# Kernel optimization log

Hardware: AMD Instinct MI355X
Metric: run time of the kernel (lower is better)

The kernel has to match this reference:

```python
import jax, jax.numpy as jnp
import numpy as np

B, S, H = 1, 4096, 3584
NQ, NKV, D = 16, 8, 256
N_REP = NQ // NKV  # GQA repeat factor = 2
WINDOW = 2048
SOFTCAP = 50.0
THETA = 10000.0
SCALE = D ** -0.5


def rotate_half(x):
    h = x.shape[-1] // 2
    return jnp.concatenate([-x[..., h:], x[..., :h]], axis=-1)


def setup_inputs() -> dict:
    key = jax.random.key(0)
    k0, k1, k2, k3, k4 = jax.random.split(key, 5)
    return {
        "hidden_states": jax.random.normal(k0, (B, S, H), jnp.float32),
        "wq": jax.random.normal(k1, (H, NQ * D), jnp.float32) / np.sqrt(H).astype(np.float32),
        "wk": jax.random.normal(k2, (H, NKV * D), jnp.float32) / np.sqrt(H).astype(np.float32),
        "wv": jax.random.normal(k3, (H, NKV * D), jnp.float32) / np.sqrt(H).astype(np.float32),
        "wo": jax.random.normal(k4, (NQ * D, H), jnp.float32) / np.sqrt(NQ * D).astype(np.float32),
        "position_ids": jnp.arange(S, dtype=jnp.int64 if jax.config.jax_enable_x64 else jnp.int32)[None, :],
    }


def reference(hidden_states, wq, wk, wv, wo, position_ids):
    b, s, h = hidden_states.shape
    # QKV projections (no bias, per attention_bias=False)
    q = (hidden_states @ wq).reshape(b, s, NQ, D).transpose(0, 2, 1, 3)   # [b, nq, s, d]
    k = (hidden_states @ wk).reshape(b, s, NKV, D).transpose(0, 2, 1, 3)  # [b, nkv, s, d]
    v = (hidden_states @ wv).reshape(b, s, NKV, D).transpose(0, 2, 1, 3)

    # Rotary embeddings (Gemma2RotaryEmbedding): freqs duplicated, rotate_half form
    pos = position_ids.astype(jnp.float32)                         # [b, s]
    inv_freq = 1.0 / (THETA ** (jnp.arange(0, D, 2, dtype=jnp.float32) / D))  # [d/2]
    freqs = pos[..., None] * inv_freq                              # [b, s, d/2]
    emb = jnp.concatenate([freqs, freqs], axis=-1)                 # [b, s, d]
    cos = jnp.cos(emb)[:, None, :, :]                              # [b, 1, s, d]
    sin = jnp.sin(emb)[:, None, :, :]
    q = q * cos + rotate_half(q) * sin
    k = k * cos + rotate_half(k) * sin

    # GQA: repeat_kv (repeat_interleave over head dim)
    k = jnp.repeat(k, N_REP, axis=1)  # [b, nq, s, d]
    v = jnp.repeat(v, N_REP, axis=1)

    # scaled scores + logit softcapping
    scores = jnp.einsum('bhqd,bhkd->bhqk', q, k) * SCALE
    scores = SOFTCAP * jnp.tanh(scores / SOFTCAP)

    # causal + sliding-window mask built from positions
    qpos = position_ids[:, None, :, None]  # [b,1,s,1]
    kpos = position_ids[:, None, None, :]  # [b,1,1,s]
    visible = (kpos <= qpos) & (kpos > qpos - WINDOW)
    scores = jnp.where(visible, scores, jnp.finfo(scores.dtype).min)

    attn = jax.nn.softmax(scores, axis=-1)
    out = jnp.einsum('bhqk,bhkd->bhqd', attn, v)      # [b, nq, s, d]
    out = out.transpose(0, 2, 1, 3).reshape(b, s, NQ * D)
    return out @ wo                                    # [b, s, h]
```

## Files before the change

### kernel.cpp

```cpp
#include <hip/hip_runtime.h>
#include <hip/hip_bf16.h>
#include <cstdint>
#include <cstddef>

#define DEVFN __device__ __forceinline__

typedef __attribute__((ext_vector_type(4))) float f32x4;
typedef __attribute__((ext_vector_type(8))) short bf16x8;
typedef __attribute__((ext_vector_type(4))) short short4v;
typedef __attribute__((ext_vector_type(8))) short short8v;

static constexpr int S = 4096;
static constexpr int H = 3584;
static constexpr int NQ = 16;
static constexpr int NKV = 8;
static constexpr int D = 256;
static constexpr int WINDOW = 2048;
static constexpr float SCALE = 0.0625f;

DEVFN unsigned short f2bf(float f) {
  union { float f; uint32_t u; } x; x.f = f;
  uint32_t u = x.u;
  u += 0x7fffu + ((u >> 16) & 1u);
  return (unsigned short)(u >> 16);
}
DEVFN float bf2f(unsigned short h) {
  union { uint32_t u; float f; } x; x.u = ((uint32_t)h) << 16;
  return x.f;
}

DEVFN void load_lds16(const void* g, void* l) {
  __builtin_amdgcn_global_load_lds((const __attribute__((address_space(1))) void*)g,
                                   (__attribute__((address_space(3))) void*)l,
                                   16, 0, 0);
}

__global__ __launch_bounds__(256) void cast_hs_kernel(const float* __restrict__ in,
                                                      unsigned short* __restrict__ out) {
  int i = (blockIdx.x * 256 + threadIdx.x) * 8;
  float4 a = *(const float4*)(in + i);
  float4 b = *(const float4*)(in + i + 4);
  short8v o;
  o[0] = (short)f2bf(a.x); o[1] = (short)f2bf(a.y);
  o[2] = (short)f2bf(a.z); o[3] = (short)f2bf(a.w);
  o[4] = (short)f2bf(b.x); o[5] = (short)f2bf(b.y);
  o[6] = (short)f2bf(b.z); o[7] = (short)f2bf(b.w);
  *(short8v*)(out + i) = o;
}

__global__ __launch_bounds__(256) void transpose_cast_kernel(const float* __restrict__ in,
                                                             unsigned short* __restrict__ out,
                                                             int rows, int cols, int out_ld) {
  __shared__ float tile[64][65];
  const int r0 = blockIdx.y * 64, c0 = blockIdx.x * 64;
  const int t = threadIdx.x;
  const int rr = t >> 4, c4 = (t & 15) * 4;
#pragma unroll
  for (int j = 0; j < 4; ++j) {
    float4 v = *(const float4*)(in + (size_t)(r0 + rr + j * 16) * cols + c0 + c4);
    tile[rr + j * 16][c4 + 0] = v.x;
    tile[rr + j * 16][c4 + 1] = v.y;
    tile[rr + j * 16][c4 + 2] = v.z;
    tile[rr + j * 16][c4 + 3] = v.w;
  }
  __syncthreads();
  const int c = t >> 2, ch = (t & 3) * 16;
  short8v o0, o1;
#pragma unroll
  for (int j = 0; j < 8; ++j) o0[j] = (short)f2bf(tile[ch + j][c]);
#pragma unroll
  for (int j = 0; j < 8; ++j) o1[j] = (short)f2bf(tile[ch + 8 + j][c]);
  unsigned short* dst = out + (size_t)(c0 + c) * out_ld + r0 + ch;
  *(short8v*)dst = o0;
  *(short8v*)(dst + 8) = o1;
}

__global__ __launch_bounds__(256) void rope_table_kernel(float* __restrict__ cs) {
  int idx = blockIdx.x * 256 + threadIdx.x;
  int s = idx >> 7, i = idx & 127;
  float inv = exp2f((float)i * -0.10381025296523007f);
  float f = (float)s * inv;
  cs[idx] = cosf(f);
  cs[(S * 128) + idx] = sinf(f);
}

DEVFN void gemm256_mainloop(const unsigned short* __restrict__ A,
                            const unsigned short* __restrict__ Bt,
                            int Kdim, int lda, int ldb, int row0, int col0,
                            char* lds, f32x4 acc[8][4]) {
  const int tid = threadIdx.x, lane = tid & 63;
  const int w = tid >> 6;
  const int wm = w >> 2, wn = w & 3;
  const int NT = Kdim >> 6;

  const int u = ((tid & 7) * 16) ^ (((tid >> 3) & 7) << 4);
  const int srow = (tid >> 3) + (u >> 6) * 128;
  const int sc = (u & 63) >> 1;

  const unsigned short* aSrc = A + (size_t)(row0 + srow) * lda + sc;
  const unsigned short* bSrc = Bt + (size_t)(col0 + srow) * ldb + sc;
  const size_t aj = (size_t)64 * lda, bj = (size_t)64 * ldb;

  char* const dA = lds + tid * 16;
  char* const dB = lds + 32768 + tid * 16;

  const int aoff = (lane & 15) * 128 + ((((lane >> 4) * 16) + wm * 64) ^ ((lane & 7) << 4));
  int boffs[4];
#pragma unroll
  for (int n = 0; n < 4; ++n)
    boffs[n] = (wn >> 1) * 8192 + ((wn & 1) * 32 + (n & 1) * 16 + (lane & 15)) * 128 +
               ((((lane >> 4) | ((n >> 1) << 2)) ^ (lane & 7)) << 4);

#define STAGE_A(kt2, kh) do { \
    char* d_ = dA + (((kt2) & 1) << 16) + ((kh) << 14); \
    const unsigned short* s_ = aSrc + (kt2) * 64 + (kh) * 32; \
    load_lds16(s_, d_); load_lds16(s_ + aj, d_ + 8192); } while (0)
#define STAGE_B(kt2, kh) do { \
    char* d_ = dB + (((kt2) & 1) << 16) + ((kh) << 14); \
    const unsigned short* s_ = bSrc + (kt2) * 64 + (kh) * 32; \
    load_lds16(s_, d_); load_lds16(s_ + bj, d_ + 8192); } while (0)

  STAGE_A(0, 0); STAGE_B(0, 0); STAGE_A(0, 1); STAGE_B(0, 1);
  if (NT > 1) { STAGE_A(1, 0); STAGE_B(1, 0); }
  asm volatile("s_waitcnt vmcnt(4)" ::: "memory");
  __builtin_amdgcn_s_barrier();
  asm volatile("" ::: "memory");

  for (int kt = 0; kt < NT; ++kt) {
    const char* lA = lds + ((kt & 1) << 16) + aoff;
    const char* lB = lds + ((kt & 1) << 16) + 32768;
    bf16x8 bfr[4];
#pragma unroll
    for (int ph = 0; ph < 4; ++ph) {
      const int kh = ph >> 1;
      const int mh = ph & 1;
      bf16x8 af[4];
#pragma unroll
      for (int j = 0; j < 4; ++j)
        af[j] = *(const bf16x8*)(lA + (kh << 14) + (mh * 4 + j) * 2048);
      if (mh == 0) {
#pragma unroll
        for (int n = 0; n < 4; ++n)
          bfr[n] = *(const bf16x8*)(lB + (kh << 14) + boffs[n]);
      }
      if (ph == 0)      { if (kt + 1 < NT) STAGE_A(kt + 1, 1); }
      else if (ph == 1) { if (kt + 1 < NT) STAGE_B(kt + 1, 1); }
      else if (ph == 2) { if (kt + 2 < NT) STAGE_A(kt + 2, 0); }
      else              { if (kt + 2 < NT) STAGE_B(kt + 2, 0); }

      asm volatile("" ::: "memory");
      __builtin_amdgcn_s_barrier();
      asm volatile("" ::: "memory");
      __builtin_amdgcn_s_setprio(1);
#pragma unroll
      for (int j = 0; j < 4; ++j)
#pragma unroll
        for (int n = 0; n < 4; ++n)
          acc[mh * 4 + j][n] =
              __builtin_amdgcn_mfma_f32_16x16x32_bf16(af[j], bfr[n], acc[mh * 4 + j][n], 0, 0, 0);
      __builtin_amdgcn_s_setprio(0);
      if (ph == 3) {
        if (kt < NT - 2) asm volatile("s_waitcnt vmcnt(4)" ::: "memory");
        else             asm volatile("s_waitcnt vmcnt(0)" ::: "memory");
      }
      asm volatile("" ::: "memory");
      __builtin_amdgcn_s_barrier();
      asm volatile("" ::: "memory");
    }
  }
#undef STAGE_A
#undef STAGE_B
}

__global__ __launch_bounds__(512, 2) void gemm_qkv_kernel(const unsigned short* __restrict__ A,
                                                          const unsigned short* __restrict__ Bt,
                                                          const float* __restrict__ cs,
                                                          unsigned short* __restrict__ qb,
                                                          unsigned short* __restrict__ kbuf,
                                                          unsigned short* __restrict__ vtb) {
  extern __shared__ char lds[];
  int bid = blockIdx.x;
  bid = (bid & 7) * 64 + (bid >> 3);
  const int bx = bid & 15, by = bid >> 4;
  const int row0 = bx * 256, col0 = by * 256;
  f32x4 acc[8][4];
  f32x4 z = {0.f, 0.f, 0.f, 0.f};
#pragma unroll
  for (int m = 0; m < 8; ++m)
#pragma unroll
    for (int n = 0; n < 4; ++n) acc[m][n] = z;

  gemm256_mainloop(A, Bt, H, H, H, row0, col0, lds, acc);

  const int lane = threadIdx.x & 63, w = threadIdx.x >> 6;
  const int wm = w >> 2, wn = w & 3;
  const int rbase = row0 + wm * 128 + (lane >> 4) * 4;

  if (col0 < 6144) {
    const bool isQ = (col0 < 4096);
    const int hoff = isQ ? (col0 >> 8) : ((col0 - 4096) >> 8);
    unsigned short* dst = isQ ? qb : kbuf;
    const int dmb = wn * 32 + (lane & 15);
#pragma unroll
    for (int m = 0; m < 8; ++m)
#pragma unroll
      for (int nl = 0; nl < 2; ++nl) {
        const int dm = dmb + nl * 16;
#pragma unroll
        for (int r = 0; r < 4; ++r) {
          const int row = rbase + m * 16 + r;
          const float c = cs[(row << 7) + dm];
          const float s = cs[(S << 7) + (row << 7) + dm];
          const float xlo = acc[m][nl][r], xhi = acc[m][nl + 2][r];
          unsigned short* p = dst + ((size_t)hoff * S + row) * D + dm;
          p[0]   = f2bf(xlo * c - xhi * s);
          p[128] = f2bf(xhi * c + xlo * s);
        }
      }
  } else {
    const int hoff = (col0 - 6144) >> 8;
#pragma unroll
    for (int m = 0; m < 8; ++m)
#pragma unroll
      for (int n = 0; n < 4; ++n) {
        const int d = wn * 32 + (n & 1) * 16 + (n >> 1) * 128 + (lane & 15);
#pragma unroll
        for (int r = 0; r < 4; ++r) {
          int row = rbase + m * 16 + r;
          vtb[((size_t)hoff * D + d) * S + row] = f2bf(acc[m][n][r]);
        }
      }
  }
}

__global__ __launch_bounds__(512, 2) void gemm_out_kernel(const unsigned short* __restrict__ A,
                                                          const unsigned short* __restrict__ Bt,
                                                          float* __restrict__ C) {
  extern __shared__ char lds[];
  int bid = blockIdx.x;
  bid = (bid & 7) * 28 + (bid >> 3);
  const int bx = bid & 15, by = bid >> 4;
  const int row0 = bx * 256, col0 = by * 256;
  f32x4 acc[8][4];
  f32x4 z = {0.f, 0.f, 0.f, 0.f};
#pragma unroll
  for (int m = 0; m < 8; ++m)
#pragma unroll
    for (int n = 0; n < 4; ++n) acc[m][n] = z;

  gemm256_mainloop(A, Bt, NQ * D, NQ * D, NQ * D, row0, col0, lds, acc);

  const int lane = threadIdx.x & 63, w = threadIdx.x >> 6;
  const int wm = w >> 2, wn = w & 3;
  const int rbase = row0 + wm * 128 + (lane >> 4) * 4;
  const int cb = col0 + wn * 32 + (lane & 15);
#pragma unroll
  for (int m = 0; m < 8; ++m)
#pragma unroll
    for (int n = 0; n < 4; ++n) {
      const int col = cb + (n & 1) * 16 + (n >> 1) * 128;
#pragma unroll
      for (int r = 0; r < 4; ++r)
        C[(size_t)(rbase + m * 16 + r) * H + col] = acc[m][n][r];
    }
}

__global__ __launch_bounds__(256, 2) void attn_kernel(const unsigned short* __restrict__ q,
                                                      const unsigned short* __restrict__ kk_,
                                                      const unsigned short* __restrict__ vt,
                                                      unsigned short* __restrict__ aout) {
  __shared__ __align__(16) char kl[2][16384];
  __shared__ __align__(16) char vl[2][16384];
  __shared__ __align__(16) char pl[8192];
  const int tid = threadIdx.x, lane = tid & 63, w = tid >> 6;
  const int h = blockIdx.y, hv = h >> 1;
  const int q0 = blockIdx.x * 128;
  const int ql = lane & 15;
  const int grp = lane >> 4;
  const int qw = q0 + w * 32;

  bf16x8 qf[2][8];
#pragma unroll
  for (int qs = 0; qs < 2; ++qs) {
    const unsigned short* qrow = q + ((size_t)h * S + qw + qs * 16 + ql) * D;
#pragma unroll
    for (int t = 0; t < 8; ++t)
      qf[qs][t] = *(const bf16x8*)(qrow + t * 32 + grp * 8);
  }

  f32x4 oacc[2][16];
  f32x4 z = {0.f, 0.f, 0.f, 0.f};
#pragma unroll
  for (int qs = 0; qs < 2; ++qs)
#pragma unroll
    for (int i = 0; i < 16; ++i) oacc[qs][i] = z;
  float lrun[2] = {0.0f, 0.0f};

  int lo = q0 - (WINDOW - 1); if (lo < 0) lo = 0;
  const int kb0 = lo & ~31;
  const int kend = q0 + 96;

  const unsigned short* kbase = kk_ + (size_t)hv * S * D;
  const unsigned short* vbase = vt + (size_t)hv * D * S;
  int koff[4], voff[4];
#pragma unroll
  for (int j = 0; j < 4; ++j) {
    int c = w + 4 * j;
    int key = c * 2 + (lane >> 5);
    int colK = (((lane & 31) * 16) ^ ((key & 7) << 4)) >> 1;
    koff[j] = key * D + colK;
    int dd = c * 16 + (lane >> 2);
    int colV = (((lane & 3) * 16) ^ (((dd >> 1) & 3) << 4)) >> 1;
    voff[j] = dd * S + colV;
  }

  auto stage = [&](int buf, int kb) {
#pragma unroll
    for (int j = 0; j < 4; ++j) {
      int c = w + 4 * j;
      load_lds16(kbase + (size_t)kb * D + koff[j], &kl[buf][c * 1024]);
      load_lds16(vbase + kb + voff[j], &vl[buf][c * 1024]);
    }
  };

  stage(0, kb0);
  int cur = 0;
  const int psw = ((ql >> 1) & 3) << 4;
  char* pw = pl + w * 2048;
  const int ksw = (ql & 7) << 4;

  for (int kb = kb0; kb <= kend; kb += 32) {
    __syncthreads();
    if (kb + 32 <= kend) stage(cur ^ 1, kb + 32);

    f32x4 sacc[2][2];
    sacc[0][0] = z; sacc[0][1] = z; sacc[1][0] = z; sacc[1][1] = z;
#pragma unroll
    for (int t = 0; t < 8; ++t) {
      bf16x8 af[2];
#pragma unroll
      for (int ms = 0; ms < 2; ++ms)
        af[ms] = *(const bf16x8*)(kl[cur] + (ms * 16 + ql) * 512 + ((t * 64 + grp * 16) ^ ksw));
#pragma unroll
      for (int qs = 0; qs < 2; ++qs)
#pragma unroll
        for (int ms = 0; ms < 2; ++ms)
          sacc[qs][ms] = __builtin_amdgcn_mfma_f32_16x16x32_bf16(af[ms], qf[qs][t], sacc[qs][ms], 0, 0, 0);
    }

#pragma unroll
    for (int qs = 0; qs < 2; ++qs) {
      const int qsb = qw + qs * 16;
      const int qg = qsb + ql;
      float pv[8];
#pragma unroll
      for (int i = 0; i < 8; ++i) {
        float y = sacc[qs][i >> 2][i & 3] * (SCALE / 50.0f);
        float y2 = y * y;
        float t = y * (15.0f + y2) * __builtin_amdgcn_rcpf(15.0f + 6.0f * y2);
        t = fminf(fmaxf(t, -1.0f), 1.0f);
        pv[i] = __expf(50.0f * t - 50.0f);
      }
      if (kb + 31 > qsb) {
#pragma unroll
        for (int i = 0; i < 8; ++i) {
          int key = kb + (i >> 2) * 16 + grp * 4 + (i & 3);
          if (key > qg) pv[i] = 0.0f;
        }
      } else if (kb < qsb - 2032) {
#pragma unroll
        for (int i = 0; i < 8; ++i) {
          int key = kb + (i >> 2) * 16 + grp * 4 + (i & 3);
          if (key <= qg - WINDOW) pv[i] = 0.0f;
        }
      }
#pragma unroll
      for (int i = 0; i < 8; ++i) lrun[qs] += pv[i];

#pragma unroll
      for (int ms = 0; ms < 2; ++ms) {
        short4v pk;
        pk[0] = (short)f2bf(pv[ms * 4 + 0]);
        pk[1] = (short)f2bf(pv[ms * 4 + 1]);
        pk[2] = (short)f2bf(pv[ms * 4 + 2]);
        pk[3] = (short)f2bf(pv[ms * 4 + 3]);
        *(short4v*)(pw + (qs * 16 + ql) * 64 + ((ms * 32 + grp * 8) ^ psw)) = pk;
      }
    }
    asm volatile("s_waitcnt lgkmcnt(0)" ::: "memory");
    bf16x8 pb[2];
#pragma unroll
    for (int qs = 0; qs < 2; ++qs)
      pb[qs] = *(const bf16x8*)(pw + (qs * 16 + ql) * 64 + ((grp * 16) ^ psw));

#pragma unroll
    for (int nt = 0; nt < 16; ++nt) {
      int dr = nt * 16 + ql;
      bf16x8 va = *(const bf16x8*)(vl[cur] + dr * 64 + ((grp * 16) ^ (((dr >> 1) & 3) << 4)));
      oacc[0][nt] = __builtin_amdgcn_mfma_f32_16x16x32_bf16(va, pb[0], oacc[0][nt], 0, 0, 0);
      oacc[1][nt] = __builtin_amdgcn_mfma_f32_16x16x32_bf16(va, pb[1], oacc[1][nt], 0, 0, 0);
    }
    cur ^= 1;
  }

#pragma unroll
  for (int qs = 0; qs < 2; ++qs) {
    float l = lrun[qs];
    l += __shfl_xor(l, 16);
    l += __shfl_xor(l, 32);
    l = fmaxf(l, 1e-35f);
    float rl = 1.0f / l;
    unsigned short* orow = aout + (size_t)(qw + qs * 16 + ql) * (NQ * D) + h * D;
#pragma unroll
    for (int nt = 0; nt < 16; ++nt) {
      short4v o;
      o[0] = (short)f2bf(oacc[qs][nt][0] * rl);
      o[1] = (short)f2bf(oacc[qs][nt][1] * rl);
      o[2] = (short)f2bf(oacc[qs][nt][2] * rl);
      o[3] = (short)f2bf(oacc[qs][nt][3] * rl);
      *(short4v*)(orow + nt * 16 + grp * 4) = o;
    }
  }
}

extern "C" void kernel_launch(void* const* d_in, const int* in_sizes, int n_in,
                              void* d_out, int out_size, void* d_ws, size_t ws_size,
                              hipStream_t stream) {
  const float* hs = (const float*)d_in[0];
  const float* wq = (const float*)d_in[1];
  const float* wk = (const float*)d_in[2];
  const float* wv = (const float*)d_in[3];
  const float* wo = (const float*)d_in[4];
  float* out = (float*)d_out;

  char* ws = (char*)d_ws;
  size_t off = 0;
  auto alloc = [&](size_t bytes) {
    char* p = ws + off;
    off += (bytes + 255) & ~(size_t)255;
    return p;
  };
  unsigned short* hsb   = (unsigned short*)alloc((size_t)S * H * 2);
  unsigned short* wqkvT = (unsigned short*)alloc((size_t)8192 * H * 2);
  unsigned short* woT   = (unsigned short*)alloc((size_t)H * 4096 * 2);
  unsigned short* qb    = (unsigned short*)alloc((size_t)NQ * S * D * 2);
  unsigned short* kbuf  = (unsigned short*)alloc((size_t)NKV * S * D * 2);
  unsigned short* vtb   = (unsigned short*)alloc((size_t)NKV * D * S * 2);
  unsigned short* aob   = (unsigned short*)alloc((size_t)S * NQ * D * 2);
  float*          cs    = (float*)alloc((size_t)S * 128 * 2 * 4);
  if (off > ws_size) return;

  cast_hs_kernel<<<(S * H) / 2048, 256, 0, stream>>>(hs, hsb);
  transpose_cast_kernel<<<dim3(4096 / 64, H / 64), 256, 0, stream>>>(wq, wqkvT, H, 4096, H);
  transpose_cast_kernel<<<dim3(2048 / 64, H / 64), 256, 0, stream>>>(wk, wqkvT + (size_t)4096 * H, H, 2048, H);
  transpose_cast_kernel<<<dim3(2048 / 64, H / 64), 256, 0, stream>>>(wv, wqkvT + (size_t)6144 * H, H, 2048, H);
  transpose_cast_kernel<<<dim3(H / 64, 4096 / 64), 256, 0, stream>>>(wo, woT, 4096, H, 4096);
  rope_table_kernel<<<(S * 128) / 256, 256, 0, stream>>>(cs);
  gemm_qkv_kernel<<<512, 512, 131072, stream>>>(hsb, wqkvT, cs, qb, kbuf, vtb);
  attn_kernel<<<dim3(S / 128, NQ), 256, 0, stream>>>(qb, kbuf, vtb, aob);
  gemm_out_kernel<<<224, 512, 131072, stream>>>(aob, woT, out);
}
```

Measured before the change: 642.7 us.

## Store V in MFMA-fragment-packed layout and read it directly from global memory

The QKV GEMM epilogue now writes V in a packed layout that matches the MFMA B-operand fragment order, one 16-byte chunk per lane per 16x32 tile. The attention kernel drops V LDS staging and its double buffer and loads V fragments straight from global memory. This removes LDS traffic and LDS footprint for V, which could raise occupancy. In exchange, V loads are not prefetched, so their latency sits on the PV MFMA critical path, relying on L2/cache hits and wave overlap to hide it.

Result: slower. 822.9 us (+28.0%).

```diff
diff --git a/kernel.cpp b/kernel.cpp
--- a/kernel.cpp
+++ b/kernel.cpp
@@ -177,7 +177,7 @@
                                                           const float* __restrict__ cs,
                                                           unsigned short* __restrict__ qb,
                                                           unsigned short* __restrict__ kbuf,
-                                                          unsigned short* __restrict__ vtb) {
+                                                          unsigned short* __restrict__ vpb) {
   extern __shared__ char lds[];
   int bid = blockIdx.x;
   bid = (bid & 7) * 64 + (bid >> 3);
@@ -218,7 +218,8 @@
         }
       }
   } else {
-    const int hoff = (col0 - 6144) >> 8;
+    const int hv_ = (col0 - 6144) >> 8;
+    unsigned short* vp = vpb + (size_t)hv_ * (S * D);
 #pragma unroll
     for (int m = 0; m < 8; ++m)
 #pragma unroll
@@ -226,8 +227,9 @@
         const int d = wn * 32 + (n & 1) * 16 + (n >> 1) * 128 + (lane & 15);
 #pragma unroll
         for (int r = 0; r < 4; ++r) {
-          int row = rbase + m * 16 + r;
-          vtb[((size_t)hoff * D + d) * S + row] = f2bf(acc[m][n][r]);
+          const int row = rbase + m * 16 + r;
+          vp[(row >> 5) * 8192 + (d >> 4) * 512 + ((row >> 3) & 3) * 128 + (d & 15) * 8 + (row & 7)]
+              = f2bf(acc[m][n][r]);
         }
       }
   }
@@ -267,10 +269,9 @@
 
 __global__ __launch_bounds__(256, 2) void attn_kernel(const unsigned short* __restrict__ q,
                                                       const unsigned short* __restrict__ kk_,
-                                                      const unsigned short* __restrict__ vt,
+                                                      const unsigned short* __restrict__ vp,
                                                       unsigned short* __restrict__ aout) {
   __shared__ __align__(16) char kl[2][16384];
-  __shared__ __align__(16) char vl[2][16384];
   __shared__ __align__(16) char pl[8192];
   const int tid = threadIdx.x, lane = tid & 63, w = tid >> 6;
   const int h = blockIdx.y, hv = h >> 1;
@@ -301,17 +302,14 @@
   const int kend = q0 + 96;
 
   const unsigned short* kbase = kk_ + (size_t)hv * S * D;
-  const unsigned short* vbase = vt + (size_t)hv * D * S;
-  int koff[4], voff[4];
+  const unsigned short* vp_h = vp + (size_t)hv * (S * D) + lane * 8;
+  int koff[4];
 #pragma unroll
   for (int j = 0; j < 4; ++j) {
     int c = w + 4 * j;
     int key = c * 2 + (lane >> 5);
     int colK = (((lane & 31) * 16) ^ ((key & 7) << 4)) >> 1;
     koff[j] = key * D + colK;
-    int dd = c * 16 + (lane >> 2);
-    int colV = (((lane & 3) * 16) ^ (((dd >> 1) & 3) << 4)) >> 1;
-    voff[j] = dd * S + colV;
   }
 
   auto stage = [&](int buf, int kb) {
@@ -319,19 +317,20 @@
     for (int j = 0; j < 4; ++j) {
       int c = w + 4 * j;
       load_lds16(kbase + (size_t)kb * D + koff[j], &kl[buf][c * 1024]);
-      load_lds16(vbase + kb + voff[j], &vl[buf][c * 1024]);
     }
   };
 
   stage(0, kb0);
   int cur = 0;
+  const int ksw = (ql & 7) << 4;
   const int psw = ((ql >> 1) & 3) << 4;
   char* pw = pl + w * 2048;
-  const int ksw = (ql & 7) << 4;
 
   for (int kb = kb0; kb <= kend; kb += 32) {
     __syncthreads();
     if (kb + 32 <= kend) stage(cur ^ 1, kb + 32);
+
+    const unsigned short* vf = vp_h + (size_t)(kb >> 5) * 8192;
 
     f32x4 sacc[2][2];
     sacc[0][0] = z; sacc[0][1] = z; sacc[1][0] = z; sacc[1][1] = z;
@@ -395,8 +394,7 @@
 
 #pragma unroll
     for (int nt = 0; nt < 16; ++nt) {
-      int dr = nt * 16 + ql;
-      bf16x8 va = *(const bf16x8*)(vl[cur] + dr * 64 + ((grp * 16) ^ (((dr >> 1) & 3) << 4)));
+      bf16x8 va = *(const bf16x8*)(vf + nt * 512);
       oacc[0][nt] = __builtin_amdgcn_mfma_f32_16x16x32_bf16(va, pb[0], oacc[0][nt], 0, 0, 0);
       oacc[1][nt] = __builtin_amdgcn_mfma_f32_16x16x32_bf16(va, pb[1], oacc[1][nt], 0, 0, 0);
     }
@@ -445,7 +443,7 @@
   unsigned short* woT   = (unsigned short*)alloc((size_t)H * 4096 * 2);
   unsigned short* qb    = (unsigned short*)alloc((size_t)NQ * S * D * 2);
   unsigned short* kbuf  = (unsigned short*)alloc((size_t)NKV * S * D * 2);
-  unsigned short* vtb   = (unsigned short*)alloc((size_t)NKV * D * S * 2);
+  unsigned short* vpb   = (unsigned short*)alloc((size_t)NKV * S * D * 2);
   unsigned short* aob   = (unsigned short*)alloc((size_t)S * NQ * D * 2);
   float*          cs    = (float*)alloc((size_t)S * 128 * 2 * 4);
   if (off > ws_size) return;
@@ -456,7 +454,7 @@
   transpose_cast_kernel<<<dim3(2048 / 64, H / 64), 256, 0, stream>>>(wv, wqkvT + (size_t)6144 * H, H, 2048, H);
   transpose_cast_kernel<<<dim3(H / 64, 4096 / 64), 256, 0, stream>>>(wo, woT, 4096, H, 4096);
   rope_table_kernel<<<(S * 128) / 256, 256, 0, stream>>>(cs);
-  gemm_qkv_kernel<<<512, 512, 131072, stream>>>(hsb, wqkvT, cs, qb, kbuf, vtb);
-  attn_kernel<<<dim3(S / 128, NQ), 256, 0, stream>>>(qb, kbuf, vtb, aob);
+  gemm_qkv_kernel<<<512, 512, 131072, stream>>>(hsb, wqkvT, cs, qb, kbuf, vpb);
+  attn_kernel<<<dim3(S / 128, NQ), 256, 0, stream>>>(qb, kbuf, vpb, aob);
   gemm_out_kernel<<<224, 512, 131072, stream>>>(aob, woT, out);
 }
```
